# Kernel optimization log

Hardware: AMD Instinct MI355X
Metric: run time of the kernel (lower is better)

The kernel has to match this reference:

```python
import jax, jax.numpy as jnp
import numpy as np

S, N, C = 16384, 2048, 8  # n_samples, n_channels, n_components

def setup_inputs() -> dict:
    key = jax.random.key(0)
    k1, k2, k3, k4 = jax.random.split(key, 4)
    return {
        "inputs": jax.random.uniform(k1, (S, N), dtype=jnp.float32),
        "components": jax.random.uniform(k2, (C, N), dtype=jnp.float32),
        "contributions": jax.random.uniform(k3, (S, C), dtype=jnp.float32),
        "shift": jax.random.normal(k4, (S, C), dtype=jnp.float32) * 3.0,
    }

def reference(inputs, components, contributions, shift):
    # fit_shift=True branch. The original builds k_matrix[i,j] = j - i and
    # coeff[i,j] = clip(1 - |shift - (j - i)|, 0, 1), then dots with the
    # component. That is exactly linear interpolation of component at
    # position i + shift, with zero padding outside [0, N-1].
    n_samples, n_channels = inputs.shape
    n_comp = components.shape[0]
    i = jnp.arange(n_channels, dtype=shift.dtype)
    pos = i[None, None, :] + shift[:, :, None]            # [S, C, N]
    j0f = jnp.floor(pos)
    frac = pos - j0f                                      # in [0, 1)
    j0 = j0f.astype(jnp.int32)
    j1 = j0 + 1
    cidx = jnp.arange(n_comp)[None, :, None]              # broadcast over [S, C, N]
    g0 = components[cidx, jnp.clip(j0, 0, n_channels - 1)]
    g1 = components[cidx, jnp.clip(j1, 0, n_channels - 1)]
    v0 = ((j0 >= 0) & (j0 < n_channels)).astype(components.dtype)
    v1 = ((j1 >= 0) & (j1 < n_channels)).astype(components.dtype)
    shifted = g0 * (1.0 - frac) * v0 + g1 * frac * v1     # [S, C, N] shifted components
    # scale by per-sample contributions and sum over components
    return jnp.einsum('scn,sc->sn', shifted, contributions)
```

## Files before the change

kernel.cpp:

```cpp
#include <hip/hip_runtime.h>
#include <hip/hip_fp16.h>


namespace {
constexpr int kS     = 16384;
constexpr int kN     = 2048;
constexpr int kC     = 8;
constexpr int kM     = 32;
constexpr int kBlock = 1024;
constexpr int kPadH  = 32;
constexpr int kUnits = 1057;
constexpr int kRowStride = 1192;

__device__ __forceinline__ int swz(int u) { return u + (u >> 3); }

__global__ __launch_bounds__(kBlock, 8)
void smf_kernel(const float* __restrict__ comps,
                const float* __restrict__ contrib,
                const float* __restrict__ shift,
                float* __restrict__ out)
{
    __shared__ uint32_t ldsU[kC * kRowStride];
    __shared__ float    ctLds[kM * kC];
    __shared__ float    shLds[kM * kC];

    const int tid = threadIdx.x;
    const int s0  = blockIdx.x * kM;

    for (int c = 0; c < kC; ++c) {
        const float* src = comps + c * kN;
        uint32_t* dst = ldsU + c * kRowStride;
        for (int u = tid; u < kUnits; u += kBlock) {
            const int j = 2 * u - kPadH;
            float2 v = make_float2(0.f, 0.f);
            if (j >= 0 && j < kN - 1) v = *reinterpret_cast<const float2*>(src + j);
            __half2 h2 = __floats2half2_rn(v.x, v.y);
            dst[swz(u)] = *reinterpret_cast<const uint32_t*>(&h2);
        }
    }

    for (int t = tid; t < (kM * kC) / 2; t += kBlock) {
        if (t < (kM * kC) / 4) {
            reinterpret_cast<float4*>(ctLds)[t] =
                reinterpret_cast<const float4*>(contrib + (size_t)s0 * kC)[t];
        } else {
            const int t2 = t - (kM * kC) / 4;
            reinterpret_cast<float4*>(shLds)[t2] =
                reinterpret_cast<const float4*>(shift + (size_t)s0 * kC)[t2];
        }
    }
    __syncthreads();

    const int q  = tid >> 8;
    const int n0 = (tid & 255) * 8;

    #pragma unroll 1
    for (int r = 0; r < kM / 4; ++r) {
        const int si = q * (kM / 4) + r;
        const int s  = s0 + si;

        const float4 ccA = *reinterpret_cast<const float4*>(ctLds + si * kC);
        const float4 ccB = *reinterpret_cast<const float4*>(ctLds + si * kC + 4);
        const float4 csA = *reinterpret_cast<const float4*>(shLds + si * kC);
        const float4 csB = *reinterpret_cast<const float4*>(shLds + si * kC + 4);

        const float ct[8] = {ccA.x, ccA.y, ccA.z, ccA.w, ccB.x, ccB.y, ccB.z, ccB.w};
        const float sh[8] = {csA.x, csA.y, csA.z, csA.w, csB.x, csB.y, csB.z, csB.w};

        float acc[8];
        #pragma unroll
        for (int k = 0; k < 8; ++k) acc[k] = 0.f;

        #pragma unroll
        for (int c = 0; c < kC; ++c) {
            const float fl = floorf(sh[c]);
            const float fr = sh[c] - fl;
            int d = (int)fl;
            d = d < -31 ? -31 : (d > 31 ? 31 : d);
            const float w1 = ct[c] * fr;
            const float w0 = ct[c] - w1;

            const int a   = n0 + d + kPadH;
            const int u0  = a >> 1;
            const bool odd = (a & 1) != 0;

            const uint32_t* row = ldsU + c * kRowStride;
            const uint32_t y0 = row[swz(u0 + 0)];
            const uint32_t y1 = row[swz(u0 + 1)];
            const uint32_t y2 = row[swz(u0 + 2)];
            const uint32_t y3 = row[swz(u0 + 3)];
            const uint32_t y4 = row[swz(u0 + 4)];
            const uint32_t y5 = row[swz(u0 + 5)];

            const uint32_t z0 = odd ? __builtin_amdgcn_alignbit(y1, y0, 16) : y0;
            const uint32_t z1 = odd ? __builtin_amdgcn_alignbit(y2, y1, 16) : y1;
            const uint32_t z2 = odd ? __builtin_amdgcn_alignbit(y3, y2, 16) : y2;
            const uint32_t z3 = odd ? __builtin_amdgcn_alignbit(y4, y3, 16) : y3;
            const uint32_t z4 = odd ? __builtin_amdgcn_alignbit(y5, y4, 16) : y4;

            const float2 f0 = __half22float2(*reinterpret_cast<const __half2*>(&z0));
            const float2 f1 = __half22float2(*reinterpret_cast<const __half2*>(&z1));
            const float2 f2 = __half22float2(*reinterpret_cast<const __half2*>(&z2));
            const float2 f3 = __half22float2(*reinterpret_cast<const __half2*>(&z3));
            const float2 f4 = __half22float2(*reinterpret_cast<const __half2*>(&z4));

            acc[0] += w0 * f0.x + w1 * f0.y;
            acc[1] += w0 * f0.y + w1 * f1.x;
            acc[2] += w0 * f1.x + w1 * f1.y;
            acc[3] += w0 * f1.y + w1 * f2.x;
            acc[4] += w0 * f2.x + w1 * f2.y;
            acc[5] += w0 * f2.y + w1 * f3.x;
            acc[6] += w0 * f3.x + w1 * f3.y;
            acc[7] += w0 * f3.y + w1 * f4.x;
        }

        float4* orow = reinterpret_cast<float4*>(out + (size_t)s * kN + n0);
        orow[0] = make_float4(acc[0], acc[1], acc[2], acc[3]);
        orow[1] = make_float4(acc[4], acc[5], acc[6], acc[7]);
    }
}
}

extern "C" void kernel_launch(void* const* d_in, const int* in_sizes, int n_in,
                              void* d_out, int out_size, void* d_ws, size_t ws_size,
                              hipStream_t stream) {
    const float* comps   = (const float*)d_in[1];
    const float* contrib = (const float*)d_in[2];
    const float* shiftp  = (const float*)d_in[3];
    float* out = (float*)d_out;

    dim3 grid(kS / kM);
    dim3 block(kBlock);
    smf_kernel<<<grid, block, 0, stream>>>(comps, contrib, shiftp, out);
}
```

Baseline: 313.4 us.

## Halve block to 512 threads and split each thread's columns into two contiguous halves

The block shrinks to 512 threads covering 16 samples, so the grid doubles. Each thread now computes 4 outputs in the first half of the row and 4 in the second half instead of 8 consecutive ones. Adjacent lanes therefore write consecutive float4s, which coalesces the global stores, and LDS reads become strided by 2 words rather than 4. The cost is that the per-block fp16 component table is rebuilt for half as many samples, doubling the LDS staging work and global component reads.

```diff
diff --git a/kernel.cpp b/kernel.cpp
--- a/kernel.cpp
+++ b/kernel.cpp
@@ -6,8 +6,8 @@
 constexpr int kS     = 16384;
 constexpr int kN     = 2048;
 constexpr int kC     = 8;
-constexpr int kM     = 32;
-constexpr int kBlock = 1024;
+constexpr int kM     = 16;
+constexpr int kBlock = 512;
 constexpr int kPadH  = 32;
 constexpr int kUnits = 1057;
 constexpr int kRowStride = 1192;
@@ -39,24 +39,24 @@
         }
     }
 
-    for (int t = tid; t < (kM * kC) / 2; t += kBlock) {
-        if (t < (kM * kC) / 4) {
-            reinterpret_cast<float4*>(ctLds)[t] =
-                reinterpret_cast<const float4*>(contrib + (size_t)s0 * kC)[t];
+    for (int tt = tid; tt < (kM * kC) / 2; tt += kBlock) {
+        if (tt < (kM * kC) / 4) {
+            reinterpret_cast<float4*>(ctLds)[tt] =
+                reinterpret_cast<const float4*>(contrib + (size_t)s0 * kC)[tt];
         } else {
-            const int t2 = t - (kM * kC) / 4;
+            const int t2 = tt - (kM * kC) / 4;
             reinterpret_cast<float4*>(shLds)[t2] =
                 reinterpret_cast<const float4*>(shift + (size_t)s0 * kC)[t2];
         }
     }
     __syncthreads();
 
-    const int q  = tid >> 8;
-    const int n0 = (tid & 255) * 8;
+    const int q = tid >> 8;
+    const int t = tid & 255;
 
     #pragma unroll 1
-    for (int r = 0; r < kM / 4; ++r) {
-        const int si = q * (kM / 4) + r;
+    for (int r = 0; r < kM / 2; ++r) {
+        const int si = q * (kM / 2) + r;
         const int s  = s0 + si;
 
         const float4 ccA = *reinterpret_cast<const float4*>(ctLds + si * kC);
@@ -67,9 +67,9 @@
         const float ct[8] = {ccA.x, ccA.y, ccA.z, ccA.w, ccB.x, ccB.y, ccB.z, ccB.w};
         const float sh[8] = {csA.x, csA.y, csA.z, csA.w, csB.x, csB.y, csB.z, csB.w};
 
-        float acc[8];
+        float accA[4], accB[4];
         #pragma unroll
-        for (int k = 0; k < 8; ++k) acc[k] = 0.f;
+        for (int k = 0; k < 4; ++k) { accA[k] = 0.f; accB[k] = 0.f; }
 
         #pragma unroll
         for (int c = 0; c < kC; ++c) {
@@ -80,43 +80,47 @@
             const float w1 = ct[c] * fr;
             const float w0 = ct[c] - w1;
 
-            const int a   = n0 + d + kPadH;
+            const int a   = 4 * t + d + kPadH;
             const int u0  = a >> 1;
             const bool odd = (a & 1) != 0;
 
             const uint32_t* row = ldsU + c * kRowStride;
-            const uint32_t y0 = row[swz(u0 + 0)];
-            const uint32_t y1 = row[swz(u0 + 1)];
-            const uint32_t y2 = row[swz(u0 + 2)];
-            const uint32_t y3 = row[swz(u0 + 3)];
-            const uint32_t y4 = row[swz(u0 + 4)];
-            const uint32_t y5 = row[swz(u0 + 5)];
+            const uint32_t yA0 = row[swz(u0 + 0)];
+            const uint32_t yA1 = row[swz(u0 + 1)];
+            const uint32_t yA2 = row[swz(u0 + 2)];
+            const uint32_t yB0 = row[swz(u0 + 512)];
+            const uint32_t yB1 = row[swz(u0 + 513)];
+            const uint32_t yB2 = row[swz(u0 + 514)];
 
-            const uint32_t z0 = odd ? __builtin_amdgcn_alignbit(y1, y0, 16) : y0;
-            const uint32_t z1 = odd ? __builtin_amdgcn_alignbit(y2, y1, 16) : y1;
-            const uint32_t z2 = odd ? __builtin_amdgcn_alignbit(y3, y2, 16) : y2;
-            const uint32_t z3 = odd ? __builtin_amdgcn_alignbit(y4, y3, 16) : y3;
-            const uint32_t z4 = odd ? __builtin_amdgcn_alignbit(y5, y4, 16) : y4;
+            const uint32_t zA0 = odd ? __builtin_amdgcn_alignbit(yA1, yA0, 16) : yA0;
+            const uint32_t zA1 = odd ? __builtin_amdgcn_alignbit(yA2, yA1, 16) : yA1;
+            const uint32_t zA2 = odd ? (yA2 >> 16) : yA2;
+            const uint32_t zB0 = odd ? __builtin_amdgcn_alignbit(yB1, yB0, 16) : yB0;
+            const uint32_t zB1 = odd ? __builtin_amdgcn_alignbit(yB2, yB1, 16) : yB1;
+            const uint32_t zB2 = odd ? (yB2 >> 16) : yB2;
 
-            const float2 f0 = __half22float2(*reinterpret_cast<const __half2*>(&z0));
-            const float2 f1 = __half22float2(*reinterpret_cast<const __half2*>(&z1));
-            const float2 f2 = __half22float2(*reinterpret_cast<const __half2*>(&z2));
-            const float2 f3 = __half22float2(*reinterpret_cast<const __half2*>(&z3));
-            const float2 f4 = __half22float2(*reinterpret_cast<const __half2*>(&z4));
+            const float2 fA0 = __half22float2(*reinterpret_cast<const __half2*>(&zA0));
+            const float2 fA1 = __half22float2(*reinterpret_cast<const __half2*>(&zA1));
+            const float2 fA2 = __half22float2(*reinterpret_cast<const __half2*>(&zA2));
+            const float2 fB0 = __half22float2(*reinterpret_cast<const __half2*>(&zB0));
+            const float2 fB1 = __half22float2(*reinterpret_cast<const __half2*>(&zB1));
+            const float2 fB2 = __half22float2(*reinterpret_cast<const __half2*>(&zB2));
 
-            acc[0] += w0 * f0.x + w1 * f0.y;
-            acc[1] += w0 * f0.y + w1 * f1.x;
-            acc[2] += w0 * f1.x + w1 * f1.y;
-            acc[3] += w0 * f1.y + w1 * f2.x;
-            acc[4] += w0 * f2.x + w1 * f2.y;
-            acc[5] += w0 * f2.y + w1 * f3.x;
-            acc[6] += w0 * f3.x + w1 * f3.y;
-            acc[7] += w0 * f3.y + w1 * f4.x;
+            accA[0] += w0 * fA0.x + w1 * fA0.y;
+            accA[1] += w0 * fA0.y + w1 * fA1.x;
+            accA[2] += w0 * fA1.x + w1 * fA1.y;
+            accA[3] += w0 * fA1.y + w1 * fA2.x;
+            accB[0] += w0 * fB0.x + w1 * fB0.y;
+            accB[1] += w0 * fB0.y + w1 * fB1.x;
+            accB[2] += w0 * fB1.x + w1 * fB1.y;
+            accB[3] += w0 * fB1.y + w1 * fB2.x;
         }
 
-        float4* orow = reinterpret_cast<float4*>(out + (size_t)s * kN + n0);
-        orow[0] = make_float4(acc[0], acc[1], acc[2], acc[3]);
-        orow[1] = make_float4(acc[4], acc[5], acc[6], acc[7]);
+        float* orow = out + (size_t)s * kN;
+        *reinterpret_cast<float4*>(orow + 4 * t) =
+            make_float4(accA[0], accA[1], accA[2], accA[3]);
+        *reinterpret_cast<float4*>(orow + 1024 + 4 * t) =
+            make_float4(accB[0], accB[1], accB[2], accB[3]);
     }
 }
 }
```

After: 285.5 us. 1.1x faster.
